# Kernel tuning notes

Hardware: AMD Instinct MI355X
Metric: run time of the kernel (lower is better)

## Reference

```python
import jax, jax.numpy as jnp
import numpy as np
import math

EMBED_DIM = 1024
NUM_HEADS = 16
HEAD_DIM = EMBED_DIM // NUM_HEADS
B, S = 2, 2048


def setup_inputs() -> dict:
    key = jax.random.key(0)
    ks = jax.random.split(key, 13)
    sc = 1.0 / math.sqrt(EMBED_DIM)
    inp = {
        "query": jax.random.normal(ks[0], (B, S, EMBED_DIM), jnp.float32),
        "key": jax.random.normal(ks[1], (B, S, EMBED_DIM), jnp.float32),
        "value": jax.random.normal(ks[2], (B, S, EMBED_DIM), jnp.float32),
        "input_patch_mask": jax.random.randint(ks[3], (B, S), 0, 2, jnp.int32),
        "Wq": jax.random.normal(ks[4], (EMBED_DIM, EMBED_DIM), jnp.float32) * sc,
        "bq": jnp.zeros((EMBED_DIM,), jnp.float32),
        "Wk": jax.random.normal(ks[5], (EMBED_DIM, EMBED_DIM), jnp.float32) * sc,
        "bk": jnp.zeros((EMBED_DIM,), jnp.float32),
        "Wv": jax.random.normal(ks[6], (EMBED_DIM, EMBED_DIM), jnp.float32) * sc,
        "bv": jnp.zeros((EMBED_DIM,), jnp.float32),
        "Wo": jax.random.normal(ks[7], (EMBED_DIM, EMBED_DIM), jnp.float32) * sc,
        "bo": jnp.zeros((EMBED_DIM,), jnp.float32),
    }
    return inp


def _masked_softmax(scores, mask):
    # Equivalent to masked_fill(-inf) -> softmax -> nan_to_num(0.0):
    # fully-masked rows produce exactly 0, without generating NaNs.
    neg_inf = jnp.array(-jnp.inf, scores.dtype)
    s = jnp.where(mask, scores, neg_inf)
    m = jnp.max(s, axis=-1, keepdims=True)
    m_safe = jnp.where(jnp.isfinite(m), m, jnp.zeros_like(m))
    e = jnp.where(mask, jnp.exp(s - m_safe), 0.0)
    denom = jnp.sum(e, axis=-1, keepdims=True)
    denom = jnp.where(denom == 0.0, 1.0, denom)
    return e / denom


def reference(query, key, value, input_patch_mask, Wq, bq, Wk, bk, Wv, bv, Wo, bo):
    b, s, d = query.shape
    h, hd = NUM_HEADS, HEAD_DIM
    q = (query @ Wq.T + bq).reshape(b, s, h, hd).transpose(0, 2, 1, 3)  # [b,h,s,hd]
    k = (key @ Wk.T + bk).reshape(b, s, h, hd).transpose(0, 2, 1, 3)
    v = (value @ Wv.T + bv).reshape(b, s, h, hd).transpose(0, 2, 1, 3)
    scores = jnp.einsum("bhqd,bhkd->bhqk", q, k) / math.sqrt(hd)
    # mask[b,i,j] = patch_mask[b,i] * patch_mask[b,j]
    mask = (input_patch_mask[:, :, None] * input_patch_mask[:, None, :]) > 0
    attn = _masked_softmax(scores, mask[:, None, :, :])  # dropout in eval mode = identity
    context = jnp.einsum("bhqk,bhkd->bhqd", attn, v)
    context = context.transpose(0, 2, 1, 3).reshape(b, s, d)
    return context @ Wo.T + bo
```

## Files before the change

### kernel.cpp

```cpp
#include <hip/hip_runtime.h>
#include <cstdint>
#include <cstddef>

#define EMBED 1024
#define NHEAD 16
#define HD    64
#define BATCH 2
#define SEQ   2048
#define MROWS (BATCH*SEQ)
#define QSCALE 0.1803368801111137f

typedef __bf16 bf16;
typedef __bf16 bf16x8 __attribute__((ext_vector_type(8)));
typedef float  f32x4  __attribute__((ext_vector_type(4)));
typedef unsigned int u32;

#if __has_builtin(__builtin_amdgcn_exp2f)
#define EXP2(x) __builtin_amdgcn_exp2f(x)
#else
#define EXP2(x) exp2f(x)
#endif

typedef const u32 __attribute__((address_space(1)))* gp_t;
typedef u32 __attribute__((address_space(3)))* lp_t;

__device__ __forceinline__ void g2l16(const void* g, void* l) {
  __builtin_amdgcn_global_load_lds((gp_t)(uintptr_t)g, (lp_t)(u32)(uintptr_t)l, 16, 0, 0);
}

#define MFMA(a, b, c) __builtin_amdgcn_mfma_f32_16x16x32_bf16((a), (b), (c), 0, 0, 0)

#define SZX8 ((MROWS*EMBED)/8)
#define SZW8 ((EMBED*EMBED)/8)

__global__ void cast_all(const float* __restrict__ q, const float* __restrict__ k,
                         const float* __restrict__ v, const float* __restrict__ wq,
                         const float* __restrict__ wk, const float* __restrict__ wv,
                         const float* __restrict__ wo,
                         bf16* xq, bf16* xk, bf16* xv,
                         bf16* wqb, bf16* wkb, bf16* wvb, bf16* wob) {
  int z = blockIdx.y;
  const float* in; bf16* out;
  switch (z) {
    case 0: in = q;  out = xq;  break;
    case 1: in = k;  out = xk;  break;
    case 2: in = v;  out = xv;  break;
    case 3: in = wq; out = wqb; break;
    case 4: in = wk; out = wkb; break;
    case 5: in = wv; out = wvb; break;
    default: in = wo; out = wob; break;
  }
  int n8 = (z < 3) ? SZX8 : SZW8;
  int i = blockIdx.x * blockDim.x + threadIdx.x;
  if (i >= n8) return;
  const float4* p = (const float4*)in;
  float4 a = p[2*i], b = p[2*i+1];
  union { bf16 h[8]; uint4 u; } r;
  r.h[0] = (bf16)a.x; r.h[1] = (bf16)a.y; r.h[2] = (bf16)a.z; r.h[3] = (bf16)a.w;
  r.h[4] = (bf16)b.x; r.h[5] = (bf16)b.y; r.h[6] = (bf16)b.z; r.h[7] = (bf16)b.w;
  ((uint4*)out)[i] = r.u;
}

#define BM 128
#define BN 128
#define BK 32
#define NKI (EMBED/BK)

__device__ __forceinline__ void gemm_core(
    const bf16* __restrict__ A, const bf16* __restrict__ W,
    int m0, int n0, bf16* Al, bf16* Bl, f32x4 (&acc)[4][4])
{
  const int tid  = threadIdx.x;
  const int lane = tid & 63, wid = tid >> 6;
  const int quad = lane >> 4, l16 = lane & 15;
  const int wm = wid >> 1, wn = wid & 1;

  const int R = tid >> 2, Cc = tid & 3;
  const int gcol = (Cc ^ ((R >> 1) & 3)) * 8;
  const bf16* Ag = A + (size_t)(m0 + R) * EMBED + gcol;
  const bf16* Bg = W + (size_t)(n0 + R) * EMBED + gcol;
  bf16* AlW = Al + wid * 512;
  bf16* BlW = Bl + wid * 512;

  g2l16(Ag, AlW);                      g2l16(Ag + (size_t)64*EMBED, AlW + 2048);
  g2l16(Bg, BlW);                      g2l16(Bg + (size_t)64*EMBED, BlW + 2048);
  __syncthreads();

  for (int ki = 0; ki < NKI; ++ki) {
    const int cur = ki & 1;
    if (ki + 1 < NKI) {
      const int nb = cur ^ 1;
      const int k0 = (ki + 1) * BK;
      g2l16(Ag + k0, AlW + nb*4096);
      g2l16(Ag + (size_t)64*EMBED + k0, AlW + nb*4096 + 2048);
      g2l16(Bg + k0, BlW + nb*4096);
      g2l16(Bg + (size_t)64*EMBED + k0, BlW + nb*4096 + 2048);
    }
    const bf16* Ac = Al + cur*4096;
    const bf16* Bc = Bl + cur*4096;
    bf16x8 af[4], bg[4];
#pragma unroll
    for (int i = 0; i < 4; ++i) {
      int ra = wm*64 + i*16 + l16;
      af[i] = *(const bf16x8*)(Ac + ra*32 + ((quad ^ ((ra>>1)&3))*8));
      int rb = wn*64 + i*16 + l16;
      bg[i] = *(const bf16x8*)(Bc + rb*32 + ((quad ^ ((rb>>1)&3))*8));
    }
#pragma unroll
    for (int i = 0; i < 4; ++i)
#pragma unroll
      for (int j = 0; j < 4; ++j)
        acc[i][j] = MFMA(af[i], bg[j], acc[i][j]);
    __syncthreads();
  }
}

__global__ __launch_bounds__(256) void qkv_kernel(
    const bf16* __restrict__ Xq, const bf16* __restrict__ Xk, const bf16* __restrict__ Xv,
    const bf16* __restrict__ Wq, const bf16* __restrict__ Wk, const bf16* __restrict__ Wv,
    const float* __restrict__ bq, const float* __restrict__ bk, const float* __restrict__ bv,
    bf16* __restrict__ Qp, bf16* __restrict__ Kp, bf16* __restrict__ VTg)
{
  __shared__ bf16 Al[2*BM*BK];
  __shared__ bf16 Bl[2*BN*BK];
  const int z = blockIdx.z;
  const bf16* A = z==0 ? Xq : z==1 ? Xk : Wv;
  const bf16* W = z==0 ? Wq : z==1 ? Wk : Xv;
  const float* bias = z==0 ? bq : z==1 ? bk : bv;
  const float scale = (z==0) ? QSCALE : 1.0f;
  const int m0 = (z < 2) ? blockIdx.y * BM : blockIdx.x * BM;
  const int n0 = (z < 2) ? blockIdx.x * BN : blockIdx.y * BN;

  f32x4 acc[4][4] = {};
  gemm_core(A, W, m0, n0, Al, Bl, acc);

  const int lane = threadIdx.x & 63, wid = threadIdx.x >> 6;
  const int quad = lane >> 4, l16 = lane & 15;
  const int wm = wid >> 1, wn = wid & 1;

#pragma unroll
  for (int i = 0; i < 4; ++i) {
#pragma unroll
    for (int j = 0; j < 4; ++j) {
      int col = n0 + wn*64 + j*16 + l16;
      if (z < 2) {
        float bv2 = bias[col];
        bf16* outp = (z == 0) ? Qp : Kp;
#pragma unroll
        for (int r = 0; r < 4; ++r) {
          int row = m0 + wm*64 + i*16 + quad*4 + r;
          outp[(size_t)row*EMBED + col] = (bf16)((acc[i][j][r] + bv2) * scale);
        }
      } else {
        int t  = col;
        int bb = t >> 11, ss = t & (SEQ-1);
        int tile = ss >> 6;
        int ppos = l16*4 + (j & 3);
#pragma unroll
        for (int r = 0; r < 4; ++r) {
          int e = m0 + wm*64 + i*16 + quad*4 + r;
          int hh = e >> 6, dd = e & (HD-1);
          VTg[(((size_t)bb*NHEAD + hh)*HD + dd)*SEQ + tile*64 + ppos]
              = (bf16)(acc[i][j][r] + bias[e]);
        }
      }
    }
  }
}

__global__ __launch_bounds__(256) void oproj_kernel(
    const bf16* __restrict__ Ctx, const bf16* __restrict__ Wo,
    const float* __restrict__ bo, float* __restrict__ out)
{
  __shared__ bf16 Al[2*128*32];
  __shared__ bf16 Bl[2*64*32];
  const int tid  = threadIdx.x;
  const int lane = tid & 63, wid = tid >> 6;
  const int quad = lane >> 4, l16 = lane & 15;
  const int m0 = blockIdx.y * 128, n0 = blockIdx.x * 64;

  const int R = tid >> 2, Cc = tid & 3;
  const int gcol = (Cc ^ ((R >> 1) & 3)) * 8;
  const bf16* Ag = Ctx + (size_t)(m0 + R) * EMBED + gcol;
  const bf16* Bg = Wo  + (size_t)(n0 + R) * EMBED + gcol;
  bf16* AlW = Al + wid * 512;
  bf16* BlW = Bl + wid * 512;

  g2l16(Ag, AlW);  g2l16(Ag + (size_t)64*EMBED, AlW + 2048);
  g2l16(Bg, BlW);
  __syncthreads();

  f32x4 acc[2][4] = {};
  for (int ki = 0; ki < NKI; ++ki) {
    const int cur = ki & 1;
    if (ki + 1 < NKI) {
      const int nb = cur ^ 1;
      const int k0 = (ki + 1) * BK;
      g2l16(Ag + k0, AlW + nb*4096);
      g2l16(Ag + (size_t)64*EMBED + k0, AlW + nb*4096 + 2048);
      g2l16(Bg + k0, BlW + nb*2048);
    }
    const bf16* Ac = Al + cur*4096;
    const bf16* Bc = Bl + cur*2048;
    bf16x8 af[2], bg[4];
#pragma unroll
    for (int u = 0; u < 2; ++u) {
      int ra = wid*32 + u*16 + l16;
      af[u] = *(const bf16x8*)(Ac + ra*32 + ((quad ^ ((ra>>1)&3))*8));
    }
#pragma unroll
    for (int j = 0; j < 4; ++j) {
      int rb = j*16 + l16;
      bg[j] = *(const bf16x8*)(Bc + rb*32 + ((quad ^ ((rb>>1)&3))*8));
    }
#pragma unroll
    for (int u = 0; u < 2; ++u)
#pragma unroll
      for (int j = 0; j < 4; ++j)
        acc[u][j] = MFMA(af[u], bg[j], acc[u][j]);
    __syncthreads();
  }

#pragma unroll
  for (int u = 0; u < 2; ++u)
#pragma unroll
    for (int j = 0; j < 4; ++j) {
      int col = n0 + j*16 + l16;
      float bv = bo[col];
#pragma unroll
      for (int r = 0; r < 4; ++r) {
        int row = m0 + wid*32 + u*16 + quad*4 + r;
        out[(size_t)row*EMBED + col] = (acc[u][j][r] + bv);
      }
    }
}

#define NT  (SEQ/64)
#define PST 72

__global__ __launch_bounds__(512, 4) void attn_kernel(
    const bf16* __restrict__ Qp, const bf16* __restrict__ Kp, const bf16* __restrict__ VT,
    const int* __restrict__ pmask, bf16* __restrict__ Ctx)
{
  __shared__ __align__(16) bf16 Kt[2][64*64];
  __shared__ __align__(16) bf16 Vt[3][64*64];
  __shared__ __align__(16) bf16 Pl[2][8][16*PST];

  const int qt = blockIdx.x, h = blockIdx.y, b = blockIdx.z;
  const int tid = threadIdx.x, lane = tid & 63, wid = tid >> 6;
  const int quad = lane >> 4, l16 = lane & 15;
  const int qrow0 = qt*128 + wid*16;

  const size_t qoff = (size_t)(b*SEQ + qrow0 + l16)*EMBED + h*HD;
  bf16x8 qf0 = *(const bf16x8*)(Qp + qoff + quad*8);
  bf16x8 qf1 = *(const bf16x8*)(Qp + qoff + 32 + quad*8);

  int qm[4];
#pragma unroll
  for (int r = 0; r < 4; ++r) qm[r] = pmask[b*SEQ + qrow0 + quad*4 + r];

  bf16 onev = (bf16)1.0f;
  bf16x8 ones = {onev, onev, onev, onev, onev, onev, onev, onev};

  const bf16* Kg  = Kp + (size_t)b*SEQ*EMBED + h*HD;
  const bf16* VTg = VT + (size_t)(b*NHEAD + h)*HD*SEQ;

  const int R = tid >> 3;
  const int Cc = tid & 7;
  const int scol = (Cc ^ (R & 7)) * 8;

  f32x4 o[4] = {};
  f32x4 lacc = {};

#define STAGE_K(kt, buf) g2l16(Kg + (size_t)((kt)*64 + R)*EMBED + scol, &Kt[buf][0] + wid*512)
#define STAGE_V(kt, buf) g2l16(VTg + (size_t)R*SEQ + (kt)*64 + scol,    &Vt[buf][0] + wid*512)

  STAGE_K(0, 0);
  STAGE_V(0, 0);
  __syncthreads();

  for (int kt = 0; kt < NT; ++kt) {
    if (kt + 1 < NT) {
      STAGE_K(kt + 1, (kt + 1) & 1);
      STAGE_V(kt + 1, (kt + 1) % 3);
    }

    const bf16* Kc = &Kt[kt & 1][0];
    f32x4 sg[4];
#pragma unroll
    for (int g = 0; g < 4; ++g) {
      int ra = g*16 + l16, sa = ra & 7;
      bf16x8 kfa = *(const bf16x8*)(Kc + ra*64 + ((quad     ^ sa)*8));
      bf16x8 kfb = *(const bf16x8*)(Kc + ra*64 + (((quad+4) ^ sa)*8));
      int km = pmask[b*SEQ + kt*64 + g*16 + l16];
      f32x4 s = {};
      s = MFMA(qf0, kfa, s);
      s = MFMA(qf1, kfb, s);
#pragma unroll
      for (int r = 0; r < 4; ++r) sg[g][r] = km ? EXP2(s[r]) : 0.0f;
    }

    if (kt > 0) {
      const bf16* Vc = &Vt[(kt - 1) % 3][0];
      bf16* Pw = &Pl[(kt - 1) & 1][wid][0];
      bf16x8 pf0 = *(const bf16x8*)(Pw + l16*PST + quad*8);
      bf16x8 pf1 = *(const bf16x8*)(Pw + l16*PST + 32 + quad*8);
      lacc = MFMA(pf0, ones, lacc);
      lacc = MFMA(pf1, ones, lacc);
#pragma unroll
      for (int t = 0; t < 4; ++t) {
        int rd = t*16 + l16, sd = rd & 7;
        bf16x8 vf0 = *(const bf16x8*)(Vc + rd*64 + ((quad     ^ sd)*8));
        bf16x8 vf1 = *(const bf16x8*)(Vc + rd*64 + (((quad+4) ^ sd)*8));
        o[t] = MFMA(pf0, vf0, o[t]);
        o[t] = MFMA(pf1, vf1, o[t]);
      }
    }

    {
      bf16* Pw = &Pl[kt & 1][wid][0];
#pragma unroll
      for (int r = 0; r < 4; ++r) {
        union { bf16 h[4]; uint2 uu; } pk;
#pragma unroll
        for (int g = 0; g < 4; ++g) pk.h[g] = (bf16)sg[g][r];
        *(uint2*)(Pw + (quad*4 + r)*PST + l16*4) = pk.uu;
      }
    }
    __syncthreads();
  }

  {
    const bf16* Vc = &Vt[(NT - 1) % 3][0];
    bf16* Pw = &Pl[(NT - 1) & 1][wid][0];
    bf16x8 pf0 = *(const bf16x8*)(Pw + l16*PST + quad*8);
    bf16x8 pf1 = *(const bf16x8*)(Pw + l16*PST + 32 + quad*8);
    lacc = MFMA(pf0, ones, lacc);
    lacc = MFMA(pf1, ones, lacc);
#pragma unroll
    for (int t = 0; t < 4; ++t) {
      int rd = t*16 + l16, sd = rd & 7;
      bf16x8 vf0 = *(const bf16x8*)(Vc + rd*64 + ((quad     ^ sd)*8));
      bf16x8 vf1 = *(const bf16x8*)(Vc + rd*64 + (((quad+4) ^ sd)*8));
      o[t] = MFMA(pf0, vf0, o[t]);
      o[t] = MFMA(pf1, vf1, o[t]);
    }
  }

  float inv[4];
#pragma unroll
  for (int r = 0; r < 4; ++r)
    inv[r] = (qm[r] && lacc[r] > 0.f) ? 1.0f / lacc[r] : 0.0f;

#pragma unroll
  for (int t = 0; t < 4; ++t)
#pragma unroll
    for (int r = 0; r < 4; ++r) {
      int row = b*SEQ + qrow0 + quad*4 + r;
      Ctx[(size_t)row*EMBED + h*HD + t*16 + l16] = (bf16)(o[t][r] * inv[r]);
    }
}

extern "C" void kernel_launch(void* const* d_in, const int* in_sizes, int n_in,
                              void* d_out, int out_size, void* d_ws, size_t ws_size,
                              hipStream_t stream)
{
  const float* query = (const float*)d_in[0];
  const float* key   = (const float*)d_in[1];
  const float* value = (const float*)d_in[2];
  const int*   pm    = (const int*)d_in[3];
  const float* Wq = (const float*)d_in[4];
  const float* bq = (const float*)d_in[5];
  const float* Wk = (const float*)d_in[6];
  const float* bk = (const float*)d_in[7];
  const float* Wv = (const float*)d_in[8];
  const float* bv = (const float*)d_in[9];
  const float* Wo = (const float*)d_in[10];
  const float* bo = (const float*)d_in[11];
  float* out = (float*)d_out;

  const size_t SZ_X = (size_t)MROWS * EMBED;
  const size_t SZ_W = (size_t)EMBED * EMBED;

  bf16* p   = (bf16*)d_ws;
  bf16* Xq  = p; p += SZ_X;
  bf16* Xk  = p; p += SZ_X;
  bf16* Xv  = p; p += SZ_X;
  bf16* Wqb = p; p += SZ_W;
  bf16* Wkb = p; p += SZ_W;
  bf16* Wvb = p; p += SZ_W;
  bf16* Wob = p; p += SZ_W;
  bf16* Qp  = p; p += SZ_X;
  bf16* Kp  = p; p += SZ_X;
  bf16* VTg = p; p += SZ_X;
  bf16* Ctx = p; p += SZ_X;

  dim3 gc((unsigned)(SZX8/256), 7);
  cast_all<<<gc, 256, 0, stream>>>(query, key, value, Wq, Wk, Wv, Wo,
                                   Xq, Xk, Xv, Wqb, Wkb, Wvb, Wob);

  dim3 gq(EMBED/BN, MROWS/BM, 3);
  qkv_kernel<<<gq, 256, 0, stream>>>(Xq, Xk, Xv, Wqb, Wkb, Wvb, bq, bk, bv, Qp, Kp, VTg);

  dim3 ga(SEQ/128, NHEAD, BATCH);
  attn_kernel<<<ga, 512, 0, stream>>>(Qp, Kp, VTg, pm, Ctx);

  dim3 gg(EMBED/64, MROWS/128);
  oproj_kernel<<<gg, 256, 0, stream>>>(Ctx, Wob, bo, out);
}
```

Before: 228.8 us.

## Give each attention wave two 16-row query tiles to reuse K/V fragments

The attention kernel drops from 512 to 256 threads per block. Each wave now handles 32 query rows as two 16-row MFMA tiles, so every K and V fragment read from LDS feeds two MFMAs. Staging loads double per thread to keep filling the same 128-row block. This cuts LDS read traffic per MFMA and loop overhead, but raises register pressure, lowers the number of waves per CU, and changes the occupancy hint.

```diff
diff --git a/kernel.cpp b/kernel.cpp
--- a/kernel.cpp
+++ b/kernel.cpp
@@ -238,26 +238,33 @@
 #define NT  (SEQ/64)
 #define PST 72
 
-__global__ __launch_bounds__(512, 4) void attn_kernel(
+__global__ __launch_bounds__(256, 2) void attn_kernel(
     const bf16* __restrict__ Qp, const bf16* __restrict__ Kp, const bf16* __restrict__ VT,
     const int* __restrict__ pmask, bf16* __restrict__ Ctx)
 {
   __shared__ __align__(16) bf16 Kt[2][64*64];
   __shared__ __align__(16) bf16 Vt[3][64*64];
-  __shared__ __align__(16) bf16 Pl[2][8][16*PST];
+  __shared__ __align__(16) bf16 Pl[2][4][32*PST];
 
   const int qt = blockIdx.x, h = blockIdx.y, b = blockIdx.z;
   const int tid = threadIdx.x, lane = tid & 63, wid = tid >> 6;
   const int quad = lane >> 4, l16 = lane & 15;
-  const int qrow0 = qt*128 + wid*16;
-
-  const size_t qoff = (size_t)(b*SEQ + qrow0 + l16)*EMBED + h*HD;
-  bf16x8 qf0 = *(const bf16x8*)(Qp + qoff + quad*8);
-  bf16x8 qf1 = *(const bf16x8*)(Qp + qoff + 32 + quad*8);
-
-  int qm[4];
-#pragma unroll
-  for (int r = 0; r < 4; ++r) qm[r] = pmask[b*SEQ + qrow0 + quad*4 + r];
+  const int qrow0 = qt*128 + wid*32;
+
+  bf16x8 qf[2][2];
+#pragma unroll
+  for (int u = 0; u < 2; ++u) {
+    const size_t qoff = (size_t)(b*SEQ + qrow0 + u*16 + l16)*EMBED + h*HD;
+    qf[u][0] = *(const bf16x8*)(Qp + qoff + quad*8);
+    qf[u][1] = *(const bf16x8*)(Qp + qoff + 32 + quad*8);
+  }
+
+  int qm[2][4];
+#pragma unroll
+  for (int u = 0; u < 2; ++u)
+#pragma unroll
+    for (int r = 0; r < 4; ++r)
+      qm[u][r] = pmask[b*SEQ + qrow0 + u*16 + quad*4 + r];
 
   bf16 onev = (bf16)1.0f;
   bf16x8 ones = {onev, onev, onev, onev, onev, onev, onev, onev};
@@ -265,15 +272,19 @@
   const bf16* Kg  = Kp + (size_t)b*SEQ*EMBED + h*HD;
   const bf16* VTg = VT + (size_t)(b*NHEAD + h)*HD*SEQ;
 
-  const int R = tid >> 3;
+  const int R  = tid >> 3;
   const int Cc = tid & 7;
   const int scol = (Cc ^ (R & 7)) * 8;
 
-  f32x4 o[4] = {};
-  f32x4 lacc = {};
-
-#define STAGE_K(kt, buf) g2l16(Kg + (size_t)((kt)*64 + R)*EMBED + scol, &Kt[buf][0] + wid*512)
-#define STAGE_V(kt, buf) g2l16(VTg + (size_t)R*SEQ + (kt)*64 + scol,    &Vt[buf][0] + wid*512)
+  f32x4 o[2][4] = {};
+  f32x4 lacc[2] = {};
+
+#define STAGE_K(kt, buf) do { \
+    g2l16(Kg + (size_t)((kt)*64 + R)*EMBED + scol,        &Kt[buf][0] + wid*512); \
+    g2l16(Kg + (size_t)((kt)*64 + R + 32)*EMBED + scol,   &Kt[buf][0] + 2048 + wid*512); } while(0)
+#define STAGE_V(kt, buf) do { \
+    g2l16(VTg + (size_t)R*SEQ + (kt)*64 + scol,           &Vt[buf][0] + wid*512); \
+    g2l16(VTg + (size_t)(R + 32)*SEQ + (kt)*64 + scol,    &Vt[buf][0] + 2048 + wid*512); } while(0)
 
   STAGE_K(0, 0);
   STAGE_V(0, 0);
@@ -286,79 +297,104 @@
     }
 
     const bf16* Kc = &Kt[kt & 1][0];
-    f32x4 sg[4];
+    f32x4 sg[2][4];
 #pragma unroll
     for (int g = 0; g < 4; ++g) {
       int ra = g*16 + l16, sa = ra & 7;
       bf16x8 kfa = *(const bf16x8*)(Kc + ra*64 + ((quad     ^ sa)*8));
       bf16x8 kfb = *(const bf16x8*)(Kc + ra*64 + (((quad+4) ^ sa)*8));
       int km = pmask[b*SEQ + kt*64 + g*16 + l16];
-      f32x4 s = {};
-      s = MFMA(qf0, kfa, s);
-      s = MFMA(qf1, kfb, s);
-#pragma unroll
-      for (int r = 0; r < 4; ++r) sg[g][r] = km ? EXP2(s[r]) : 0.0f;
+      f32x4 s0 = {}, s1 = {};
+      s0 = MFMA(qf[0][0], kfa, s0);
+      s0 = MFMA(qf[0][1], kfb, s0);
+      s1 = MFMA(qf[1][0], kfa, s1);
+      s1 = MFMA(qf[1][1], kfb, s1);
+#pragma unroll
+      for (int r = 0; r < 4; ++r) {
+        sg[0][g][r] = km ? EXP2(s0[r]) : 0.0f;
+        sg[1][g][r] = km ? EXP2(s1[r]) : 0.0f;
+      }
     }
 
     if (kt > 0) {
       const bf16* Vc = &Vt[(kt - 1) % 3][0];
-      bf16* Pw = &Pl[(kt - 1) & 1][wid][0];
-      bf16x8 pf0 = *(const bf16x8*)(Pw + l16*PST + quad*8);
-      bf16x8 pf1 = *(const bf16x8*)(Pw + l16*PST + 32 + quad*8);
-      lacc = MFMA(pf0, ones, lacc);
-      lacc = MFMA(pf1, ones, lacc);
+      const bf16* Pw = &Pl[(kt - 1) & 1][wid][0];
+      bf16x8 pf[2][2];
+#pragma unroll
+      for (int u = 0; u < 2; ++u) {
+        pf[u][0] = *(const bf16x8*)(Pw + (u*16 + l16)*PST + quad*8);
+        pf[u][1] = *(const bf16x8*)(Pw + (u*16 + l16)*PST + 32 + quad*8);
+        lacc[u] = MFMA(pf[u][0], ones, lacc[u]);
+        lacc[u] = MFMA(pf[u][1], ones, lacc[u]);
+      }
 #pragma unroll
       for (int t = 0; t < 4; ++t) {
         int rd = t*16 + l16, sd = rd & 7;
         bf16x8 vf0 = *(const bf16x8*)(Vc + rd*64 + ((quad     ^ sd)*8));
         bf16x8 vf1 = *(const bf16x8*)(Vc + rd*64 + (((quad+4) ^ sd)*8));
-        o[t] = MFMA(pf0, vf0, o[t]);
-        o[t] = MFMA(pf1, vf1, o[t]);
+#pragma unroll
+        for (int u = 0; u < 2; ++u) {
+          o[u][t] = MFMA(pf[u][0], vf0, o[u][t]);
+          o[u][t] = MFMA(pf[u][1], vf1, o[u][t]);
+        }
       }
     }
 
     {
       bf16* Pw = &Pl[kt & 1][wid][0];
 #pragma unroll
-      for (int r = 0; r < 4; ++r) {
-        union { bf16 h[4]; uint2 uu; } pk;
-#pragma unroll
-        for (int g = 0; g < 4; ++g) pk.h[g] = (bf16)sg[g][r];
-        *(uint2*)(Pw + (quad*4 + r)*PST + l16*4) = pk.uu;
-      }
+      for (int u = 0; u < 2; ++u)
+#pragma unroll
+        for (int r = 0; r < 4; ++r) {
+          union { bf16 h[4]; uint2 uu; } pk;
+#pragma unroll
+          for (int g = 0; g < 4; ++g) pk.h[g] = (bf16)sg[u][g][r];
+          *(uint2*)(Pw + (u*16 + quad*4 + r)*PST + l16*4) = pk.uu;
+        }
     }
     __syncthreads();
   }
 
   {
     const bf16* Vc = &Vt[(NT - 1) % 3][0];
-    bf16* Pw = &Pl[(NT - 1) & 1][wid][0];
-    bf16x8 pf0 = *(const bf16x8*)(Pw + l16*PST + quad*8);
-    bf16x8 pf1 = *(const bf16x8*)(Pw + l16*PST + 32 + quad*8);
-    lacc = MFMA(pf0, ones, lacc);
-    lacc = MFMA(pf1, ones, lacc);
+    const bf16* Pw = &Pl[(NT - 1) & 1][wid][0];
+    bf16x8 pf[2][2];
+#pragma unroll
+    for (int u = 0; u < 2; ++u) {
+      pf[u][0] = *(const bf16x8*)(Pw + (u*16 + l16)*PST + quad*8);
+      pf[u][1] = *(const bf16x8*)(Pw + (u*16 + l16)*PST + 32 + quad*8);
+      lacc[u] = MFMA(pf[u][0], ones, lacc[u]);
+      lacc[u] = MFMA(pf[u][1], ones, lacc[u]);
+    }
 #pragma unroll
     for (int t = 0; t < 4; ++t) {
       int rd = t*16 + l16, sd = rd & 7;
       bf16x8 vf0 = *(const bf16x8*)(Vc + rd*64 + ((quad     ^ sd)*8));
       bf16x8 vf1 = *(const bf16x8*)(Vc + rd*64 + (((quad+4) ^ sd)*8));
-      o[t] = MFMA(pf0, vf0, o[t]);
-      o[t] = MFMA(pf1, vf1, o[t]);
-    }
-  }
-
-  float inv[4];
-#pragma unroll
-  for (int r = 0; r < 4; ++r)
-    inv[r] = (qm[r] && lacc[r] > 0.f) ? 1.0f / lacc[r] : 0.0f;
-
-#pragma unroll
-  for (int t = 0; t < 4; ++t)
-#pragma unroll
-    for (int r = 0; r < 4; ++r) {
-      int row = b*SEQ + qrow0 + quad*4 + r;
-      Ctx[(size_t)row*EMBED + h*HD + t*16 + l16] = (bf16)(o[t][r] * inv[r]);
-    }
+#pragma unroll
+      for (int u = 0; u < 2; ++u) {
+        o[u][t] = MFMA(pf[u][0], vf0, o[u][t]);
+        o[u][t] = MFMA(pf[u][1], vf1, o[u][t]);
+      }
+    }
+  }
+
+  float inv[2][4];
+#pragma unroll
+  for (int u = 0; u < 2; ++u)
+#pragma unroll
+    for (int r = 0; r < 4; ++r)
+      inv[u][r] = (qm[u][r] && lacc[u][r] > 0.f) ? 1.0f / lacc[u][r] : 0.0f;
+
+#pragma unroll
+  for (int u = 0; u < 2; ++u)
+#pragma unroll
+    for (int t = 0; t < 4; ++t)
+#pragma unroll
+      for (int r = 0; r < 4; ++r) {
+        int row = b*SEQ + qrow0 + u*16 + quad*4 + r;
+        Ctx[(size_t)row*EMBED + h*HD + t*16 + l16] = (bf16)(o[u][t][r] * inv[u][r]);
+      }
 }
 
 extern "C" void kernel_launch(void* const* d_in, const int* in_sizes, int n_in,
@@ -403,7 +439,7 @@
   qkv_kernel<<<gq, 256, 0, stream>>>(Xq, Xk, Xv, Wqb, Wkb, Wvb, bq, bk, bv, Qp, Kp, VTg);
 
   dim3 ga(SEQ/128, NHEAD, BATCH);
-  attn_kernel<<<ga, 512, 0, stream>>>(Qp, Kp, VTg, pm, Ctx);
+  attn_kernel<<<ga, 256, 0, stream>>>(Qp, Kp, VTg, pm, Ctx);
 
   dim3 gg(EMBED/64, MROWS/128);
   oproj_kernel<<<gg, 256, 0, stream>>>(Ctx, Wob, bo, out);
```

Measured after the change: 231.9 us. No clear change (+1.4%).

## Keep attention probabilities in registers via transposed QK MFMA; vectorize V-projection stores

Applied to the files above, without the earlier changes.

The QK^T MFMA now takes its operands in swapped order (K as A, Q as B), so each lane's exp'd scores already match the A-operand layout of the PV MFMA. The probabilities are packed into bf16x8 registers directly, and the LDS P buffer with its store/load round trip goes away. The permuted V-tile positions are rearranged so this register layout lines up. The key mask is loaded as int4 per quad, and occupancy bounds are relaxed from 4 to 2 blocks per SM to leave room for registers. The V-projection epilogue now writes packed 4-element bf16 stores with a vectorized bias load instead of scalar scattered stores.

```diff
diff --git a/kernel.cpp b/kernel.cpp
--- a/kernel.cpp
+++ b/kernel.cpp
@@ -138,12 +138,12 @@
   const int quad = lane >> 4, l16 = lane & 15;
   const int wm = wid >> 1, wn = wid & 1;
 
-#pragma unroll
-  for (int i = 0; i < 4; ++i) {
-#pragma unroll
-    for (int j = 0; j < 4; ++j) {
-      int col = n0 + wn*64 + j*16 + l16;
-      if (z < 2) {
+  if (z < 2) {
+#pragma unroll
+    for (int i = 0; i < 4; ++i) {
+#pragma unroll
+      for (int j = 0; j < 4; ++j) {
+        int col = n0 + wn*64 + j*16 + l16;
         float bv2 = bias[col];
         bf16* outp = (z == 0) ? Qp : Kp;
 #pragma unroll
@@ -151,18 +151,26 @@
           int row = m0 + wm*64 + i*16 + quad*4 + r;
           outp[(size_t)row*EMBED + col] = (bf16)((acc[i][j][r] + bv2) * scale);
         }
-      } else {
-        int t  = col;
-        int bb = t >> 11, ss = t & (SEQ-1);
-        int tile = ss >> 6;
-        int ppos = l16*4 + (j & 3);
-#pragma unroll
-        for (int r = 0; r < 4; ++r) {
-          int e = m0 + wm*64 + i*16 + quad*4 + r;
-          int hh = e >> 6, dd = e & (HD-1);
-          VTg[(((size_t)bb*NHEAD + hh)*HD + dd)*SEQ + tile*64 + ppos]
-              = (bf16)(acc[i][j][r] + bias[e]);
-        }
+      }
+    }
+  } else {
+    const int tcol0 = n0 + wn*64;
+    const int bb   = tcol0 >> 11;
+    const int tile = (tcol0 & (SEQ-1)) >> 6;
+    const int rA = l16 & 3, qA = l16 >> 2;
+    const int pbase = (rA>>1)*32 + qA*8 + (rA&1)*4;
+#pragma unroll
+    for (int i = 0; i < 4; ++i) {
+      float4 bv4 = *(const float4*)&bias[m0 + wm*64 + i*16 + quad*4];
+#pragma unroll
+      for (int r = 0; r < 4; ++r) {
+        int e = m0 + wm*64 + i*16 + quad*4 + r;
+        int hh = e >> 6, dd = e & (HD-1);
+        float bvr = (r==0) ? bv4.x : (r==1) ? bv4.y : (r==2) ? bv4.z : bv4.w;
+        union { bf16 h[4]; uint2 uu; } pk;
+#pragma unroll
+        for (int j = 0; j < 4; ++j) pk.h[j] = (bf16)(acc[i][j][r] + bvr);
+        *(uint2*)&VTg[(((size_t)bb*NHEAD + hh)*HD + dd)*SEQ + tile*64 + pbase] = pk.uu;
       }
     }
   }
@@ -236,15 +244,13 @@
 }
 
 #define NT  (SEQ/64)
-#define PST 72
-
-__global__ __launch_bounds__(512, 4) void attn_kernel(
+
+__global__ __launch_bounds__(512, 2) void attn_kernel(
     const bf16* __restrict__ Qp, const bf16* __restrict__ Kp, const bf16* __restrict__ VT,
     const int* __restrict__ pmask, bf16* __restrict__ Ctx)
 {
   __shared__ __align__(16) bf16 Kt[2][64*64];
   __shared__ __align__(16) bf16 Vt[3][64*64];
-  __shared__ __align__(16) bf16 Pl[2][8][16*PST];
 
   const int qt = blockIdx.x, h = blockIdx.y, b = blockIdx.z;
   const int tid = threadIdx.x, lane = tid & 63, wid = tid >> 6;
@@ -264,6 +270,7 @@
 
   const bf16* Kg  = Kp + (size_t)b*SEQ*EMBED + h*HD;
   const bf16* VTg = VT + (size_t)(b*NHEAD + h)*HD*SEQ;
+  const int*  kmb = pmask + b*SEQ;
 
   const int R = tid >> 3;
   const int Cc = tid & 7;
@@ -271,6 +278,7 @@
 
   f32x4 o[4] = {};
   f32x4 lacc = {};
+  bf16x8 pa0 = {}, pa1 = {};
 
 #define STAGE_K(kt, buf) g2l16(Kg + (size_t)((kt)*64 + R)*EMBED + scol, &Kt[buf][0] + wid*512)
 #define STAGE_V(kt, buf) g2l16(VTg + (size_t)R*SEQ + (kt)*64 + scol,    &Vt[buf][0] + wid*512)
@@ -292,58 +300,49 @@
       int ra = g*16 + l16, sa = ra & 7;
       bf16x8 kfa = *(const bf16x8*)(Kc + ra*64 + ((quad     ^ sa)*8));
       bf16x8 kfb = *(const bf16x8*)(Kc + ra*64 + (((quad+4) ^ sa)*8));
-      int km = pmask[b*SEQ + kt*64 + g*16 + l16];
+      int4 kq = *(const int4*)(kmb + kt*64 + g*16 + quad*4);
       f32x4 s = {};
-      s = MFMA(qf0, kfa, s);
-      s = MFMA(qf1, kfb, s);
-#pragma unroll
-      for (int r = 0; r < 4; ++r) sg[g][r] = km ? EXP2(s[r]) : 0.0f;
+      s = MFMA(kfa, qf0, s);
+      s = MFMA(kfb, qf1, s);
+      sg[g][0] = kq.x ? EXP2(s[0]) : 0.0f;
+      sg[g][1] = kq.y ? EXP2(s[1]) : 0.0f;
+      sg[g][2] = kq.z ? EXP2(s[2]) : 0.0f;
+      sg[g][3] = kq.w ? EXP2(s[3]) : 0.0f;
     }
 
     if (kt > 0) {
       const bf16* Vc = &Vt[(kt - 1) % 3][0];
-      bf16* Pw = &Pl[(kt - 1) & 1][wid][0];
-      bf16x8 pf0 = *(const bf16x8*)(Pw + l16*PST + quad*8);
-      bf16x8 pf1 = *(const bf16x8*)(Pw + l16*PST + 32 + quad*8);
-      lacc = MFMA(pf0, ones, lacc);
-      lacc = MFMA(pf1, ones, lacc);
+      lacc = MFMA(pa0, ones, lacc);
+      lacc = MFMA(pa1, ones, lacc);
 #pragma unroll
       for (int t = 0; t < 4; ++t) {
         int rd = t*16 + l16, sd = rd & 7;
         bf16x8 vf0 = *(const bf16x8*)(Vc + rd*64 + ((quad     ^ sd)*8));
         bf16x8 vf1 = *(const bf16x8*)(Vc + rd*64 + (((quad+4) ^ sd)*8));
-        o[t] = MFMA(pf0, vf0, o[t]);
-        o[t] = MFMA(pf1, vf1, o[t]);
+        o[t] = MFMA(pa0, vf0, o[t]);
+        o[t] = MFMA(pa1, vf1, o[t]);
       }
     }
 
-    {
-      bf16* Pw = &Pl[kt & 1][wid][0];
-#pragma unroll
-      for (int r = 0; r < 4; ++r) {
-        union { bf16 h[4]; uint2 uu; } pk;
-#pragma unroll
-        for (int g = 0; g < 4; ++g) pk.h[g] = (bf16)sg[g][r];
-        *(uint2*)(Pw + (quad*4 + r)*PST + l16*4) = pk.uu;
-      }
-    }
+    pa0[0] = (bf16)sg[0][0]; pa0[1] = (bf16)sg[1][0]; pa0[2] = (bf16)sg[2][0]; pa0[3] = (bf16)sg[3][0];
+    pa0[4] = (bf16)sg[0][1]; pa0[5] = (bf16)sg[1][1]; pa0[6] = (bf16)sg[2][1]; pa0[7] = (bf16)sg[3][1];
+    pa1[0] = (bf16)sg[0][2]; pa1[1] = (bf16)sg[1][2]; pa1[2] = (bf16)sg[2][2]; pa1[3] = (bf16)sg[3][2];
+    pa1[4] = (bf16)sg[0][3]; pa1[5] = (bf16)sg[1][3]; pa1[6] = (bf16)sg[2][3]; pa1[7] = (bf16)sg[3][3];
+
     __syncthreads();
   }
 
   {
     const bf16* Vc = &Vt[(NT - 1) % 3][0];
-    bf16* Pw = &Pl[(NT - 1) & 1][wid][0];
-    bf16x8 pf0 = *(const bf16x8*)(Pw + l16*PST + quad*8);
-    bf16x8 pf1 = *(const bf16x8*)(Pw + l16*PST + 32 + quad*8);
-    lacc = MFMA(pf0, ones, lacc);
-    lacc = MFMA(pf1, ones, lacc);
+    lacc = MFMA(pa0, ones, lacc);
+    lacc = MFMA(pa1, ones, lacc);
 #pragma unroll
     for (int t = 0; t < 4; ++t) {
       int rd = t*16 + l16, sd = rd & 7;
       bf16x8 vf0 = *(const bf16x8*)(Vc + rd*64 + ((quad     ^ sd)*8));
       bf16x8 vf1 = *(const bf16x8*)(Vc + rd*64 + (((quad+4) ^ sd)*8));
-      o[t] = MFMA(pf0, vf0, o[t]);
-      o[t] = MFMA(pf1, vf1, o[t]);
+      o[t] = MFMA(pa0, vf0, o[t]);
+      o[t] = MFMA(pa1, vf1, o[t]);
     }
   }
 
```

Result: slower. 234.2 us (+2.4%).
